# Optimization experiments

Hardware: AMD Instinct MI355X
Metric: run time of the kernel (lower is better)

Reference implementation:

```python
import jax, jax.numpy as jnp
import numpy as np

V, D, NL = 50257, 768, 12
DI, DS, DC, DTR = 1536, 16, 4, 48  # d_inner, d_state, d_conv, dt_rank
B, S = 2, 1024


def _mamba_layer(x, iw, cw, cb, xw, dw, db, Alog, Dp, ow):
    # x: (B,S,D)
    xz = x @ iw.T                      # (B,S,2*DI)
    xin, z = jnp.split(xz, 2, axis=-1)
    # depthwise causal conv over sequence
    xc = jax.lax.conv_general_dilated(
        jnp.transpose(xin, (0, 2, 1)), cw[:, None, :],
        window_strides=(1,), padding=[(DC - 1, 0)],
        feature_group_count=DI, dimension_numbers=('NCL', 'OIL', 'NCL'))
    xin = jax.nn.silu(jnp.transpose(xc, (0, 2, 1)) + cb)  # (B,S,DI)
    dbl = xin @ xw.T                   # (B,S,DTR+2*DS)
    dt, Bm, Cm = dbl[..., :DTR], dbl[..., DTR:DTR + DS], dbl[..., DTR + DS:]
    dt = jax.nn.softplus(dt @ dw.T + db)  # (B,S,DI)
    A = -jnp.exp(Alog)                 # (DI,DS)

    def step(h, inp):
        dt_t, B_t, C_t, x_t = inp      # (B,DI),(B,DS),(B,DS),(B,DI)
        h = h * jnp.exp(dt_t[:, :, None] * A) + (dt_t * x_t)[:, :, None] * B_t[:, None, :]
        y = jnp.einsum('bds,bs->bd', h, C_t)
        return h, y

    h0 = jnp.zeros((x.shape[0], DI, DS), dtype=x.dtype)
    xs = (jnp.transpose(dt, (1, 0, 2)), jnp.transpose(Bm, (1, 0, 2)),
          jnp.transpose(Cm, (1, 0, 2)), jnp.transpose(xin, (1, 0, 2)))
    _, ys = jax.lax.scan(step, h0, xs)
    y = jnp.transpose(ys, (1, 0, 2)) + xin * Dp  # (B,S,DI)
    y = y * jax.nn.silu(z)
    return y @ ow.T                    # (B,S,D)


def _layernorm(x, w, b):
    mu = jnp.mean(x, axis=-1, keepdims=True)
    var = jnp.mean(jnp.square(x - mu), axis=-1, keepdims=True)
    return (x - mu) * jax.lax.rsqrt(var + 1e-5) * w + b


def setup_inputs() -> dict:
    key = jax.random.key(0)
    ks = jax.random.split(key, 10)
    s = 0.02
    input_ids = jax.random.randint(ks[0], (B, S), 0, V)
    emb = jax.random.normal(ks[1], (V, D), jnp.float32) * s
    in_proj_w = jax.random.normal(ks[2], (NL, 2 * DI, D), jnp.float32) * s
    conv_w = jax.random.normal(ks[3], (NL, DI, DC), jnp.float32) * 0.2
    conv_b = jnp.zeros((NL, DI), jnp.float32)
    x_proj_w = jax.random.normal(ks[4], (NL, DTR + 2 * DS, DI), jnp.float32) * s
    dt_proj_w = jax.random.normal(ks[5], (NL, DI, DTR), jnp.float32) * (DTR ** -0.5)
    dt_proj_b = jax.random.normal(ks[6], (NL, DI), jnp.float32) * 0.1 - 4.0
    A_log = jnp.broadcast_to(jnp.log(jnp.arange(1, DS + 1, dtype=jnp.float32)), (NL, DI, DS)) + 0.0
    D_param = jnp.ones((NL, DI), jnp.float32)
    out_proj_w = jax.random.normal(ks[7], (NL, D, DI), jnp.float32) * s
    norm_w = jnp.ones((D,), jnp.float32)
    norm_b = jnp.zeros((D,), jnp.float32)
    return {"input_ids": input_ids, "emb": emb, "in_proj_w": in_proj_w,
            "conv_w": conv_w, "conv_b": conv_b, "x_proj_w": x_proj_w,
            "dt_proj_w": dt_proj_w, "dt_proj_b": dt_proj_b, "A_log": A_log,
            "D_param": D_param, "out_proj_w": out_proj_w,
            "norm_w": norm_w, "norm_b": norm_b}


def reference(input_ids, emb, in_proj_w, conv_w, conv_b, x_proj_w, dt_proj_w,
              dt_proj_b, A_log, D_param, out_proj_w, norm_w, norm_b):
    x = emb[input_ids] * (D ** 0.5)    # (B,S,D)
    for i in range(NL):
        x = _mamba_layer(x, in_proj_w[i], conv_w[i], conv_b[i], x_proj_w[i],
                         dt_proj_w[i], dt_proj_b[i], A_log[i], D_param[i], out_proj_w[i])
    x = _layernorm(x, norm_w, norm_b)
    return x @ emb.T                   # tied lm_head: (B,S,V)
```

## Files before the change

### kernel.cpp

```cpp
#include <hip/hip_runtime.h>
#include <hip/hip_bf16.h>

#define DI 1536
#define DS 16
#define DC 4
#define DTR 48
#define NB 2
#define SL 1024
#define DM 768
#define NLAYER 12
#define VOCAB 50257
#define ROWS (NB*SL)
#define CCH 32
#define CLEN (SL/CCH)
#define NBIG (DI+32)

typedef __attribute__((ext_vector_type(8))) short bf16x8;
typedef __attribute__((ext_vector_type(4))) short short4v;
typedef __attribute__((ext_vector_type(4))) float f32x4;

__device__ inline short f2bf(float f) {
    unsigned u = __builtin_bit_cast(unsigned, f);
    unsigned r = (u + 0x7fffu + ((u >> 16) & 1u)) >> 16;
    return (short)r;
}
__device__ inline float bf2f(unsigned short u) {
    unsigned x = ((unsigned)u) << 16;
    return __builtin_bit_cast(float, x);
}

__device__ __forceinline__ void gl_lds16(const void* g, void* l) {
    __builtin_amdgcn_global_load_lds(
        (const __attribute__((address_space(1))) unsigned int*)g,
        (__attribute__((address_space(3))) unsigned int*)l, 16, 0, 0);
}

__global__ __launch_bounds__(256) void cvt_bf16_k(const float* __restrict__ src,
                                                  unsigned short* __restrict__ dst,
                                                  int n4) {
    int i = blockIdx.x * 256 + threadIdx.x;
    if (i >= n4) return;
    float4 v = *reinterpret_cast<const float4*>(src + (size_t)i * 4);
    short4v o;
    o[0] = f2bf(v.x); o[1] = f2bf(v.y); o[2] = f2bf(v.z); o[3] = f2bf(v.w);
    *reinterpret_cast<short4v*>(dst + (size_t)i * 4) = o;
}

__global__ __launch_bounds__(256) void wc_k(
    const float* __restrict__ dtw_all,
    const float* __restrict__ xpw_all,
    unsigned short* __restrict__ wbig)
{
    int l = blockIdx.z;
    const float* dtw = dtw_all + (size_t)l * DI * DTR;
    const float* xpw = xpw_all + (size_t)l * 80 * DI;
    unsigned short* wb = wbig + (size_t)l * NBIG * DI;
    int tid = threadIdx.x;
    if (blockIdx.y == 12) {
        if (blockIdx.x == 0) {
            for (int idx = tid; idx < 32 * DI; idx += 256) {
                int rr = idx / DI, k = idx - rr * DI;
                wb[(size_t)(DI + rr) * DI + k] =
                    (unsigned short)f2bf(xpw[(size_t)(48 + rr) * DI + k]);
            }
        }
        return;
    }
    __shared__ float sd[128 * 48];
    __shared__ float sx[48 * 128];
    int d0 = blockIdx.y * 128, k0 = blockIdx.x * 128;
    for (int idx = tid; idx < 128 * 48; idx += 256) {
        int r = idx / 48, j = idx - r * 48;
        sd[idx] = dtw[(size_t)(d0 + r) * DTR + j];
    }
    for (int idx = tid; idx < 48 * 128; idx += 256) {
        int j = idx / 128, k = idx - j * 128;
        sx[idx] = xpw[(size_t)j * DI + k0 + k];
    }
    __syncthreads();
    int tx = tid & 15, ty = tid >> 4;
    float acc[8][8] = {};
    for (int j = 0; j < 48; ++j) {
        float a[8], w[8];
        #pragma unroll
        for (int i = 0; i < 8; ++i) a[i] = sd[(ty * 8 + i) * 48 + j];
        #pragma unroll
        for (int i = 0; i < 8; ++i) w[i] = sx[j * 128 + tx * 8 + i];
        #pragma unroll
        for (int i = 0; i < 8; ++i)
            #pragma unroll
            for (int jj = 0; jj < 8; ++jj)
                acc[i][jj] += a[i] * w[jj];
    }
    for (int i = 0; i < 8; ++i)
        for (int jj = 0; jj < 8; ++jj)
            wb[(size_t)(d0 + ty * 8 + i) * DI + k0 + tx * 8 + jj] =
                (unsigned short)f2bf(acc[i][jj]);
}

__global__ __launch_bounds__(256) void embed_k(const int* __restrict__ ids,
                                               const float* __restrict__ emb,
                                               unsigned short* __restrict__ xbf) {
    int i = blockIdx.x * 256 + threadIdx.x;
    if (i >= ROWS * (DM / 4)) return;
    int row = i / (DM / 4);
    int c4 = (i - row * (DM / 4)) * 4;
    float4 v = *reinterpret_cast<const float4*>(
        &emb[(size_t)ids[row] * DM + c4]);
    const float s = 27.712812921102035f;
    short4v o;
    o[0] = f2bf(v.x * s); o[1] = f2bf(v.y * s);
    o[2] = f2bf(v.z * s); o[3] = f2bf(v.w * s);
    *reinterpret_cast<short4v*>(&xbf[(size_t)row * DM + c4]) = o;
}

template<int MT, int NBUF, int OUT, bool NTST>
__global__ __launch_bounds__(256) void gemm_bf16(
    const unsigned short* __restrict__ A, int lda,
    const unsigned short* __restrict__ W, int ldw,
    float* __restrict__ C, unsigned short* __restrict__ Cbf, int ldc,
    int GY, int N, int K,
    const float* __restrict__ bias, float* __restrict__ aux)
{
    constexpr int BKT = 32;
    constexpr int CPR = BKT / 8;
    constexpr int ACA = (MT * CPR + 255) / 256;
    constexpr int ACW = 128 * CPR / 256;
    constexpr int ISS = ACA + ACW;
    constexpr int MFR = MT / 32;
    constexpr int BUFS = (MT + 128) * BKT;
    __shared__ __align__(16) short smem[NBUF * BUFS];

    const int tid  = threadIdx.x;
    const int lane = tid & 63;
    const int wid  = tid >> 6;
    const int wr   = wid >> 1, wc = wid & 1;

    const int nwg = gridDim.x;
    const int q = nwg >> 3, rm = nwg & 7;
    const int xcd = blockIdx.x & 7, bidx = blockIdx.x >> 3;
    const int wg = (xcd < rm ? xcd * (q + 1) : rm * (q + 1) + (xcd - rm) * q) + bidx;
    const int row0 = (wg % GY) * MT;
    const int col0 = (wg / GY) * 128;

    const unsigned short* gA[ACA];
    const unsigned short* gW[ACW];
    #pragma unroll
    for (int i = 0; i < ACA; ++i) {
        int cid = i * 256 + ((MT == 32) ? (tid & 127) : tid);
        int r = cid / CPR, c = cid % CPR;
        gA[i] = A + (size_t)(row0 + r) * lda + ((c ^ ((r >> 1) & 3)) * 8);
    }
    #pragma unroll
    for (int i = 0; i < ACW; ++i) {
        int cid = i * 256 + tid;
        int r = cid / CPR, c = cid % CPR;
        int rg = col0 + r; if (rg > N - 1) rg = N - 1;
        gW[i] = W + (size_t)rg * ldw + ((c ^ ((r >> 1) & 3)) * 8);
    }

    const int arow = (MT == 32 ? wr * 16 : wr * (MT / 2)) + (lane & 15);
    const int brow = wc * 64 + (lane & 15);
    const int szA = (arow >> 1) & 3;
    const int szB = (brow >> 1) & 3;
    const int hi = lane >> 4;

    auto STAGE = [&](int buf) {
        short* As = smem + buf * BUFS;
        short* Ws = As + MT * BKT;
        #pragma unroll
        for (int i = 0; i < ACA; ++i) {
            int cbase = (MT == 32) ? ((wid & 1) * 64) : (i * 256 + wid * 64);
            gl_lds16(gA[i], &As[cbase * 8]);
            gA[i] += BKT;
        }
        #pragma unroll
        for (int i = 0; i < ACW; ++i) {
            gl_lds16(gW[i], &Ws[(i * 256 + wid * 64) * 8]);
            gW[i] += BKT;
        }
    };

    f32x4 acc[MFR][4] = {};

    const int ntiles = K / BKT;
    #pragma unroll
    for (int p = 0; p < NBUF - 1; ++p) STAGE(p);

    for (int t = 0; t < ntiles; ++t) {
        const int next = t + NBUF - 1;
        if (next < ntiles) STAGE(next % NBUF);
        int ahead = ntiles - 1 - t;
        if (ahead > NBUF - 1) ahead = NBUF - 1;
        if (NBUF == 3 && ahead == 2)
            asm volatile("s_waitcnt vmcnt(%0)" :: "n"(2 * ISS) : "memory");
        else if (ahead == 1)
            asm volatile("s_waitcnt vmcnt(%0)" :: "n"(ISS) : "memory");
        else if (ahead == 0)
            asm volatile("s_waitcnt vmcnt(0)" ::: "memory");
        __builtin_amdgcn_sched_barrier(0);
        __builtin_amdgcn_s_barrier();

        const short* As = smem + (t % NBUF) * BUFS;
        const short* Ws = As + MT * BKT;
        bf16x8 a[MFR], b[4];
        #pragma unroll
        for (int mf = 0; mf < MFR; ++mf)
            a[mf] = *reinterpret_cast<const bf16x8*>(
                &As[(arow + mf * 16) * BKT + ((hi ^ szA) * 8)]);
        #pragma unroll
        for (int nf = 0; nf < 4; ++nf)
            b[nf] = *reinterpret_cast<const bf16x8*>(
                &Ws[(brow + nf * 16) * BKT + ((hi ^ szB) * 8)]);
        #pragma unroll
        for (int mf = 0; mf < MFR; ++mf)
            #pragma unroll
            for (int nf = 0; nf < 4; ++nf)
                acc[mf][nf] = __builtin_amdgcn_mfma_f32_16x16x32_bf16(
                    a[mf], b[nf], acc[mf][nf], 0, 0, 0);

        __builtin_amdgcn_s_barrier();
    }

    if (OUT == 0 && NTST) {
        __syncthreads();
        float* Cs = (float*)smem;
        #pragma unroll
        for (int mf = 0; mf < MFR; ++mf) {
            __syncthreads();
            #pragma unroll
            for (int nf = 0; nf < 4; ++nf) {
                #pragma unroll
                for (int j = 0; j < 4; ++j)
                    Cs[(wr * 16 + hi * 4 + j) * 132 + wc * 64 + nf * 16 + (lane & 15)]
                        = acc[mf][nf][j];
            }
            __syncthreads();
            #pragma unroll
            for (int rr = 0; rr < 8; ++rr) {
                int lrow = wid * 8 + rr;
                int grow = row0 + (lrow < 16 ? mf * 16 + lrow
                                             : (MT / 2) + mf * 16 + (lrow - 16));
                #pragma unroll
                for (int hf = 0; hf < 2; ++hf) {
                    int cc = col0 + hf * 64 + lane;
                    if (cc < N)
                        __builtin_nontemporal_store(
                            Cs[lrow * 132 + hf * 64 + lane],
                            &C[(size_t)grow * ldc + cc]);
                }
            }
        }
    } else {
        #pragma unroll
        for (int mf = 0; mf < MFR; ++mf) {
            #pragma unroll
            for (int nf = 0; nf < 4; ++nf) {
                int r  = row0 + (MT == 32 ? wr * 16 : wr * (MT / 2)) + mf * 16 + hi * 4;
                int cc = col0 + wc * 64 + nf * 16 + (lane & 15);
                if (cc < N) {
                    f32x4 d = acc[mf][nf];
                    if (OUT == 3) {
                        if (cc < DI) {
                            float bv = bias[cc];
                            #pragma unroll
                            for (int j = 0; j < 4; ++j) {
                                float v = d[j] + bv;
                                v = (v > 20.f) ? v : log1pf(__expf(v));
                                Cbf[(size_t)(r + j) * ldc + cc] = (unsigned short)f2bf(v);
                            }
                        } else {
                            #pragma unroll
                            for (int j = 0; j < 4; ++j)
                                aux[(size_t)(r + j) * 32 + (cc - DI)] = d[j];
                        }
                    } else if (OUT == 2) {
                        #pragma unroll
                        for (int j = 0; j < 4; ++j)
                            Cbf[(size_t)(r + j) * ldc + cc] = (unsigned short)f2bf(d[j]);
                    } else {
                        #pragma unroll
                        for (int j = 0; j < 4; ++j)
                            C[(size_t)(r + j) * ldc + cc] = d[j];
                    }
                }
            }
        }
    }
}

__global__ __launch_bounds__(256) void conv_silu_k(
    const unsigned short* __restrict__ xz, const float* __restrict__ cw,
    const float* __restrict__ cb, unsigned short* __restrict__ xinb)
{
    int i = blockIdx.x * 256 + threadIdx.x;
    if (i >= ROWS * (DI / 8)) return;
    int row = i / (DI / 8);
    int c = (i - row * (DI / 8)) * 8;
    int t = row & (SL - 1);
    int b = row >> 10;

    float4 wv[8];
    float accv[8];
    #pragma unroll
    for (int j = 0; j < 8; ++j) {
        wv[j] = *reinterpret_cast<const float4*>(&cw[(c + j) * DC]);
        accv[j] = cb[c + j];
    }
    const unsigned short* base = xz + ((size_t)(b * SL)) * (2 * DI) + c;
    #pragma unroll
    for (int k = 0; k < DC; ++k) {
        int tt = t + k - (DC - 1);
        if (tt >= 0) {
            bf16x8 v = *reinterpret_cast<const bf16x8*>(
                &base[(size_t)tt * (2 * DI)]);
            #pragma unroll
            for (int j = 0; j < 8; ++j)
                accv[j] += bf2f((unsigned short)v[j]) *
                           reinterpret_cast<const float*>(&wv[j])[k];
        }
    }
    bf16x8 o;
    #pragma unroll
    for (int j = 0; j < 8; ++j) {
        float v = accv[j] / (1.f + __expf(-accv[j]));
        o[j] = f2bf(v);
    }
    *reinterpret_cast<bf16x8*>(&xinb[(size_t)row * DI + c]) = o;
}

__global__ __launch_bounds__(256) void scan_phase1(
    const unsigned short* __restrict__ dt,
    const float* __restrict__ bc,
    const unsigned short* __restrict__ xin,
    const float* __restrict__ Alog,
    float* __restrict__ hend,
    float* __restrict__ eprod)
{
    int blk = blockIdx.x;
    int c = blk % CCH;
    int tmp = blk / CCH;
    int dblk = tmp % (DI / 16);
    int b = tmp / (DI / 16);
    int s = threadIdx.x & 15;
    int d = dblk * 16 + (threadIdx.x >> 4);
    float A = -__expf(Alog[d * DS + s]);
    float h = 0.f, P = 1.f;
    const int rowbase = b * SL + c * CLEN;
    #pragma unroll 4
    for (int t = 0; t < CLEN; ++t) {
        int r = rowbase + t;
        float dtv = bf2f(dt[(size_t)r * DI + d]);
        float xv  = bf2f(xin[(size_t)r * DI + d]);
        float Bv  = bc[(size_t)r * 32 + s];
        float e = __expf(dtv * A);
        h = h * e + dtv * xv * Bv;
        P *= e;
    }
    size_t idx = ((size_t)(b * CCH + c) * DI + d) * DS + s;
    hend[idx]  = h;
    eprod[idx] = P;
}

__global__ __launch_bounds__(256) void scan_phase3(
    const unsigned short* __restrict__ dt,
    const float* __restrict__ bc,
    const unsigned short* __restrict__ xin,
    const unsigned short* __restrict__ xz,
    const float* __restrict__ Alog,
    const float* __restrict__ Dp,
    const float* __restrict__ hend,
    const float* __restrict__ eprod,
    unsigned short* __restrict__ ybf)
{
    int blk = blockIdx.x;
    int c = blk % CCH;
    int tmp = blk / CCH;
    int dblk = tmp % (DI / 16);
    int b = tmp / (DI / 16);
    int s = threadIdx.x & 15;
    int d = dblk * 16 + (threadIdx.x >> 4);
    float A = -__expf(Alog[d * DS + s]);
    float Dv = Dp[d];

    float h = 0.f;
    const size_t pbase = ((size_t)b * CCH * DI + d) * DS + s;
    for (int j = 0; j < c; ++j) {
        size_t idx = pbase + (size_t)j * (DI * DS);
        h = h * eprod[idx] + hend[idx];
    }

    const int rowbase = b * SL + c * CLEN;
    #pragma unroll 2
    for (int t = 0; t < CLEN; ++t) {
        int r = rowbase + t;
        float dtv = bf2f(dt[(size_t)r * DI + d]);
        float xv  = bf2f(xin[(size_t)r * DI + d]);
        float Bv  = bc[(size_t)r * 32 + s];
        float Cv  = bc[(size_t)r * 32 + 16 + s];
        float e = __expf(dtv * A);
        h = h * e + dtv * xv * Bv;
        float p = h * Cv;
        p += __shfl_xor(p, 1, 64);
        p += __shfl_xor(p, 2, 64);
        p += __shfl_xor(p, 4, 64);
        p += __shfl_xor(p, 8, 64);
        if (s == 0) {
            float z = bf2f(xz[(size_t)r * (2 * DI) + DI + d]);
            float yv = (p + xv * Dv) * (z / (1.f + __expf(-z)));
            ybf[(size_t)r * DI + d] = (unsigned short)f2bf(yv);
        }
    }
}

__global__ __launch_bounds__(256) void ln_k(
    const unsigned short* __restrict__ x, const float* __restrict__ w,
    const float* __restrict__ b, unsigned short* __restrict__ o)
{
    int row = blockIdx.x;
    int tid = threadIdx.x;
    const unsigned short* xr = x + (size_t)row * DM;
    float v0 = bf2f(xr[tid]), v1 = bf2f(xr[tid + 256]), v2 = bf2f(xr[tid + 512]);
    float s = v0 + v1 + v2;
    #pragma unroll
    for (int off = 1; off < 64; off <<= 1) s += __shfl_xor(s, off, 64);
    __shared__ float red[4];
    __shared__ float red2[4];
    int wid = tid >> 6, lane = tid & 63;
    if (lane == 0) red[wid] = s;
    __syncthreads();
    float mu = (red[0] + red[1] + red[2] + red[3]) * (1.f / 768.f);
    float d0 = v0 - mu, d1 = v1 - mu, d2 = v2 - mu;
    float q = d0 * d0 + d1 * d1 + d2 * d2;
    #pragma unroll
    for (int off = 1; off < 64; off <<= 1) q += __shfl_xor(q, off, 64);
    if (lane == 0) red2[wid] = q;
    __syncthreads();
    float var = (red2[0] + red2[1] + red2[2] + red2[3]) * (1.f / 768.f);
    float rs = rsqrtf(var + 1e-5f);
    o[(size_t)row * DM + tid]       = (unsigned short)f2bf(d0 * rs * w[tid]       + b[tid]);
    o[(size_t)row * DM + tid + 256] = (unsigned short)f2bf(d1 * rs * w[tid + 256] + b[tid + 256]);
    o[(size_t)row * DM + tid + 512] = (unsigned short)f2bf(d2 * rs * w[tid + 512] + b[tid + 512]);
}

extern "C" void kernel_launch(void* const* d_in, const int* in_sizes, int n_in,
                              void* d_out, int out_size, void* d_ws, size_t ws_size,
                              hipStream_t stream) {
    const int*   ids        = (const int*)d_in[0];
    const float* emb        = (const float*)d_in[1];
    const float* in_proj_w  = (const float*)d_in[2];
    const float* conv_w     = (const float*)d_in[3];
    const float* conv_b     = (const float*)d_in[4];
    const float* x_proj_w   = (const float*)d_in[5];
    const float* dt_proj_w  = (const float*)d_in[6];
    const float* dt_proj_b  = (const float*)d_in[7];
    const float* A_log      = (const float*)d_in[8];
    const float* D_param    = (const float*)d_in[9];
    const float* out_proj_w = (const float*)d_in[10];
    const float* norm_w     = (const float*)d_in[11];
    const float* norm_b     = (const float*)d_in[12];
    float* out = (float*)d_out;

    char* base = (char*)d_ws;
    size_t off = 0;
    auto alloc_f = [&](size_t n) { float* p = (float*)(base + off); off += n * 4; return p; };
    auto alloc_u = [&](size_t n) { unsigned short* p = (unsigned short*)(base + off); off += n * 2; return p; };

    float* bc    = alloc_f((size_t)ROWS * 32);
    float* hend  = alloc_f((size_t)NB * CCH * DI * DS);
    float* eprod = alloc_f((size_t)NB * CCH * DI * DS);
    unsigned short* xbf   = alloc_u((size_t)ROWS * DM);
    unsigned short* xzb   = alloc_u((size_t)ROWS * 2 * DI);
    unsigned short* xinb  = alloc_u((size_t)ROWS * DI);
    unsigned short* dtbf  = alloc_u((size_t)ROWS * DI);
    unsigned short* ybf   = alloc_u((size_t)ROWS * DI);
    unsigned short* xlnbf = alloc_u((size_t)ROWS * DM);
    unsigned short* inw_bf = alloc_u((size_t)NLAYER * 2 * DI * DM);
    unsigned short* ow_bf  = alloc_u((size_t)NLAYER * DM * DI);
    unsigned short* wbig  = alloc_u((size_t)NLAYER * NBIG * DI);
    unsigned short* emb_bf = alloc_u((size_t)VOCAB * DM);
    (void)ws_size;

    {
        int n4a = NLAYER * 2 * DI * DM / 4;
        cvt_bf16_k<<<(n4a + 255) / 256, 256, 0, stream>>>(in_proj_w, inw_bf, n4a);
        int n4b = NLAYER * DM * DI / 4;
        cvt_bf16_k<<<(n4b + 255) / 256, 256, 0, stream>>>(out_proj_w, ow_bf, n4b);
        wc_k<<<dim3(12, 13, NLAYER), 256, 0, stream>>>(dt_proj_w, x_proj_w, wbig);
        int n4e = VOCAB * DM / 4;
        cvt_bf16_k<<<(n4e + 255) / 256, 256, 0, stream>>>(emb, emb_bf, n4e);
    }

    embed_k<<<(ROWS * (DM / 4) + 255) / 256, 256, 0, stream>>>(ids, emb, xbf);

    const int scan_grid = NB * (DI / 16) * CCH;

    for (int i = 0; i < NLAYER; ++i) {
        const float* cw  = conv_w  + (size_t)i * DI * DC;
        const float* cb  = conv_b  + (size_t)i * DI;
        const float* dtb = dt_proj_b + (size_t)i * DI;
        const float* Al  = A_log   + (size_t)i * DI * DS;
        const float* Dpar= D_param + (size_t)i * DI;

        const unsigned short* inw = inw_bf + (size_t)i * 2 * DI * DM;
        gemm_bf16<64, 3, 2, false><<<24 * 32, 256, 0, stream>>>(
            xbf, DM, inw, DM, nullptr, xzb, 2 * DI, 32, 2 * DI, DM, nullptr, nullptr);

        conv_silu_k<<<(ROWS * (DI / 8)) / 256, 256, 0, stream>>>(xzb, cw, cb, xinb);

        const unsigned short* wb = wbig + (size_t)i * NBIG * DI;
        gemm_bf16<64, 3, 3, false><<<13 * 32, 256, 0, stream>>>(
            xinb, DI, wb, DI, nullptr, dtbf, DI, 32, NBIG, DI, dtb, bc);

        scan_phase1<<<scan_grid, 256, 0, stream>>>(dtbf, bc, xinb, Al, hend, eprod);
        scan_phase3<<<scan_grid, 256, 0, stream>>>(dtbf, bc, xinb, xzb, Al, Dpar,
                                                   hend, eprod, ybf);

        const unsigned short* ow = ow_bf + (size_t)i * DM * DI;
        gemm_bf16<32, 3, 2, false><<<64 * 6, 256, 0, stream>>>(
            ybf, DI, ow, DI, nullptr, xbf, DM, 64, DM, DI, nullptr, nullptr);
    }

    ln_k<<<ROWS, 256, 0, stream>>>(xbf, norm_w, norm_b, xlnbf);
    gemm_bf16<128, 2, 0, true><<<393 * 16, 256, 0, stream>>>(
        xlnbf, DM, emb_bf, DM, out, nullptr, VOCAB, 16, VOCAB, DM, nullptr, nullptr);
}
```

Measured before the change: 3.130 ms.

## Widen lm_head GEMM tile, shuffle-broadcast scan inputs, merge weight conversions

The GEMM kernel gains an NCOL template parameter, and the final vocabulary projection now uses 128x256 tiles to raise reuse of the A operand, at the cost of more accumulator registers and LDS. Both scan phases now load dt, x and z once per 16 timesteps, one value per lane, and broadcast them with wave shuffles instead of having all 16 state lanes reload the same values each step. The three fp32-to-bf16 weight conversion launches are merged into a single kernel to cut launch overhead.

```diff
diff --git a/kernel.cpp b/kernel.cpp
--- a/kernel.cpp
+++ b/kernel.cpp
@@ -35,11 +35,17 @@
         (__attribute__((address_space(3))) unsigned int*)l, 16, 0, 0);
 }
 
-__global__ __launch_bounds__(256) void cvt_bf16_k(const float* __restrict__ src,
-                                                  unsigned short* __restrict__ dst,
-                                                  int n4) {
+__global__ __launch_bounds__(256) void cvt3_k(
+    const float* __restrict__ s0, unsigned short* __restrict__ d0, int n40,
+    const float* __restrict__ s1, unsigned short* __restrict__ d1, int n41,
+    const float* __restrict__ s2, unsigned short* __restrict__ d2, int n42)
+{
     int i = blockIdx.x * 256 + threadIdx.x;
-    if (i >= n4) return;
+    const float* src; unsigned short* dst;
+    if (i < n40) { src = s0; dst = d0; }
+    else if (i < n40 + n41) { i -= n40; src = s1; dst = d1; }
+    else if (i < n40 + n41 + n42) { i -= n40 + n41; src = s2; dst = d2; }
+    else return;
     float4 v = *reinterpret_cast<const float4*>(src + (size_t)i * 4);
     short4v o;
     o[0] = f2bf(v.x); o[1] = f2bf(v.y); o[2] = f2bf(v.z); o[3] = f2bf(v.w);
@@ -114,7 +120,7 @@
     *reinterpret_cast<short4v*>(&xbf[(size_t)row * DM + c4]) = o;
 }
 
-template<int MT, int NBUF, int OUT, bool NTST>
+template<int MT, int NCOL, int NBUF, int OUT, bool NTST>
 __global__ __launch_bounds__(256) void gemm_bf16(
     const unsigned short* __restrict__ A, int lda,
     const unsigned short* __restrict__ W, int ldw,
@@ -125,10 +131,11 @@
     constexpr int BKT = 32;
     constexpr int CPR = BKT / 8;
     constexpr int ACA = (MT * CPR + 255) / 256;
-    constexpr int ACW = 128 * CPR / 256;
+    constexpr int ACW = NCOL * CPR / 256;
     constexpr int ISS = ACA + ACW;
     constexpr int MFR = MT / 32;
-    constexpr int BUFS = (MT + 128) * BKT;
+    constexpr int NFR = NCOL / 32;
+    constexpr int BUFS = (MT + NCOL) * BKT;
     __shared__ __align__(16) short smem[NBUF * BUFS];
 
     const int tid  = threadIdx.x;
@@ -141,7 +148,7 @@
     const int xcd = blockIdx.x & 7, bidx = blockIdx.x >> 3;
     const int wg = (xcd < rm ? xcd * (q + 1) : rm * (q + 1) + (xcd - rm) * q) + bidx;
     const int row0 = (wg % GY) * MT;
-    const int col0 = (wg / GY) * 128;
+    const int col0 = (wg / GY) * NCOL;
 
     const unsigned short* gA[ACA];
     const unsigned short* gW[ACW];
@@ -160,7 +167,7 @@
     }
 
     const int arow = (MT == 32 ? wr * 16 : wr * (MT / 2)) + (lane & 15);
-    const int brow = wc * 64 + (lane & 15);
+    const int brow = wc * (NCOL / 2) + (lane & 15);
     const int szA = (arow >> 1) & 3;
     const int szB = (brow >> 1) & 3;
     const int hi = lane >> 4;
@@ -181,7 +188,7 @@
         }
     };
 
-    f32x4 acc[MFR][4] = {};
+    f32x4 acc[MFR][NFR] = {};
 
     const int ntiles = K / BKT;
     #pragma unroll
@@ -203,19 +210,19 @@
 
         const short* As = smem + (t % NBUF) * BUFS;
         const short* Ws = As + MT * BKT;
-        bf16x8 a[MFR], b[4];
+        bf16x8 a[MFR], b[NFR];
         #pragma unroll
         for (int mf = 0; mf < MFR; ++mf)
             a[mf] = *reinterpret_cast<const bf16x8*>(
                 &As[(arow + mf * 16) * BKT + ((hi ^ szA) * 8)]);
         #pragma unroll
-        for (int nf = 0; nf < 4; ++nf)
+        for (int nf = 0; nf < NFR; ++nf)
             b[nf] = *reinterpret_cast<const bf16x8*>(
                 &Ws[(brow + nf * 16) * BKT + ((hi ^ szB) * 8)]);
         #pragma unroll
         for (int mf = 0; mf < MFR; ++mf)
             #pragma unroll
-            for (int nf = 0; nf < 4; ++nf)
+            for (int nf = 0; nf < NFR; ++nf)
                 acc[mf][nf] = __builtin_amdgcn_mfma_f32_16x16x32_bf16(
                     a[mf], b[nf], acc[mf][nf], 0, 0, 0);
 
@@ -224,15 +231,16 @@
 
     if (OUT == 0 && NTST) {
         __syncthreads();
+        constexpr int CSLD = NCOL + 4;
         float* Cs = (float*)smem;
         #pragma unroll
         for (int mf = 0; mf < MFR; ++mf) {
             __syncthreads();
             #pragma unroll
-            for (int nf = 0; nf < 4; ++nf) {
+            for (int nf = 0; nf < NFR; ++nf) {
                 #pragma unroll
                 for (int j = 0; j < 4; ++j)
-                    Cs[(wr * 16 + hi * 4 + j) * 132 + wc * 64 + nf * 16 + (lane & 15)]
+                    Cs[(wr * 16 + hi * 4 + j) * CSLD + wc * (NCOL / 2) + nf * 16 + (lane & 15)]
                         = acc[mf][nf][j];
             }
             __syncthreads();
@@ -242,11 +250,11 @@
                 int grow = row0 + (lrow < 16 ? mf * 16 + lrow
                                              : (MT / 2) + mf * 16 + (lrow - 16));
                 #pragma unroll
-                for (int hf = 0; hf < 2; ++hf) {
+                for (int hf = 0; hf < NCOL / 64; ++hf) {
                     int cc = col0 + hf * 64 + lane;
                     if (cc < N)
                         __builtin_nontemporal_store(
-                            Cs[lrow * 132 + hf * 64 + lane],
+                            Cs[lrow * CSLD + hf * 64 + lane],
                             &C[(size_t)grow * ldc + cc]);
                 }
             }
@@ -255,9 +263,9 @@
         #pragma unroll
         for (int mf = 0; mf < MFR; ++mf) {
             #pragma unroll
-            for (int nf = 0; nf < 4; ++nf) {
+            for (int nf = 0; nf < NFR; ++nf) {
                 int r  = row0 + (MT == 32 ? wr * 16 : wr * (MT / 2)) + mf * 16 + hi * 4;
-                int cc = col0 + wc * 64 + nf * 16 + (lane & 15);
+                int cc = col0 + wc * (NCOL / 2) + nf * 16 + (lane & 15);
                 if (cc < N) {
                     f32x4 d = acc[mf][nf];
                     if (OUT == 3) {
@@ -342,20 +350,28 @@
     int tmp = blk / CCH;
     int dblk = tmp % (DI / 16);
     int b = tmp / (DI / 16);
-    int s = threadIdx.x & 15;
+    int lane = threadIdx.x & 63;
+    int s = lane & 15;
+    int g = lane & 0x30;
     int d = dblk * 16 + (threadIdx.x >> 4);
     float A = -__expf(Alog[d * DS + s]);
     float h = 0.f, P = 1.f;
     const int rowbase = b * SL + c * CLEN;
-    #pragma unroll 4
-    for (int t = 0; t < CLEN; ++t) {
-        int r = rowbase + t;
-        float dtv = bf2f(dt[(size_t)r * DI + d]);
-        float xv  = bf2f(xin[(size_t)r * DI + d]);
-        float Bv  = bc[(size_t)r * 32 + s];
-        float e = __expf(dtv * A);
-        h = h * e + dtv * xv * Bv;
-        P *= e;
+    #pragma unroll
+    for (int half = 0; half < 2; ++half) {
+        int rb = rowbase + half * 16;
+        int rl = rb + s;
+        float dtv_b = bf2f(dt[(size_t)rl * DI + d]);
+        float xv_b  = bf2f(xin[(size_t)rl * DI + d]);
+        #pragma unroll
+        for (int t = 0; t < 16; ++t) {
+            float dtv = __shfl(dtv_b, g | t, 64);
+            float xv  = __shfl(xv_b,  g | t, 64);
+            float Bv  = bc[(size_t)(rb + t) * 32 + s];
+            float e = __expf(dtv * A);
+            h = h * e + dtv * xv * Bv;
+            P *= e;
+        }
     }
     size_t idx = ((size_t)(b * CCH + c) * DI + d) * DS + s;
     hend[idx]  = h;
@@ -378,7 +394,9 @@
     int tmp = blk / CCH;
     int dblk = tmp % (DI / 16);
     int b = tmp / (DI / 16);
-    int s = threadIdx.x & 15;
+    int lane = threadIdx.x & 63;
+    int s = lane & 15;
+    int g = lane & 0x30;
     int d = dblk * 16 + (threadIdx.x >> 4);
     float A = -__expf(Alog[d * DS + s]);
     float Dv = Dp[d];
@@ -391,24 +409,32 @@
     }
 
     const int rowbase = b * SL + c * CLEN;
-    #pragma unroll 2
-    for (int t = 0; t < CLEN; ++t) {
-        int r = rowbase + t;
-        float dtv = bf2f(dt[(size_t)r * DI + d]);
-        float xv  = bf2f(xin[(size_t)r * DI + d]);
-        float Bv  = bc[(size_t)r * 32 + s];
-        float Cv  = bc[(size_t)r * 32 + 16 + s];
-        float e = __expf(dtv * A);
-        h = h * e + dtv * xv * Bv;
-        float p = h * Cv;
-        p += __shfl_xor(p, 1, 64);
-        p += __shfl_xor(p, 2, 64);
-        p += __shfl_xor(p, 4, 64);
-        p += __shfl_xor(p, 8, 64);
-        if (s == 0) {
-            float z = bf2f(xz[(size_t)r * (2 * DI) + DI + d]);
-            float yv = (p + xv * Dv) * (z / (1.f + __expf(-z)));
-            ybf[(size_t)r * DI + d] = (unsigned short)f2bf(yv);
+    #pragma unroll
+    for (int half = 0; half < 2; ++half) {
+        int rb = rowbase + half * 16;
+        int rl = rb + s;
+        float dtv_b = bf2f(dt[(size_t)rl * DI + d]);
+        float xv_b  = bf2f(xin[(size_t)rl * DI + d]);
+        float zv_b  = bf2f(xz[(size_t)rl * (2 * DI) + DI + d]);
+        #pragma unroll
+        for (int t = 0; t < 16; ++t) {
+            float dtv = __shfl(dtv_b, g | t, 64);
+            float xv  = __shfl(xv_b,  g | t, 64);
+            int r = rb + t;
+            float Bv  = bc[(size_t)r * 32 + s];
+            float Cv  = bc[(size_t)r * 32 + 16 + s];
+            float e = __expf(dtv * A);
+            h = h * e + dtv * xv * Bv;
+            float p = h * Cv;
+            p += __shfl_xor(p, 1, 64);
+            p += __shfl_xor(p, 2, 64);
+            p += __shfl_xor(p, 4, 64);
+            p += __shfl_xor(p, 8, 64);
+            float z = __shfl(zv_b, g | t, 64);
+            if (s == 0) {
+                float yv = (p + xv * Dv) * (z / (1.f + __expf(-z)));
+                ybf[(size_t)r * DI + d] = (unsigned short)f2bf(yv);
+            }
         }
     }
 }
@@ -483,12 +509,12 @@
 
     {
         int n4a = NLAYER * 2 * DI * DM / 4;
-        cvt_bf16_k<<<(n4a + 255) / 256, 256, 0, stream>>>(in_proj_w, inw_bf, n4a);
         int n4b = NLAYER * DM * DI / 4;
-        cvt_bf16_k<<<(n4b + 255) / 256, 256, 0, stream>>>(out_proj_w, ow_bf, n4b);
+        int n4e = VOCAB * DM / 4;
+        int n4t = n4a + n4b + n4e;
+        cvt3_k<<<(n4t + 255) / 256, 256, 0, stream>>>(
+            in_proj_w, inw_bf, n4a, out_proj_w, ow_bf, n4b, emb, emb_bf, n4e);
         wc_k<<<dim3(12, 13, NLAYER), 256, 0, stream>>>(dt_proj_w, x_proj_w, wbig);
-        int n4e = VOCAB * DM / 4;
-        cvt_bf16_k<<<(n4e + 255) / 256, 256, 0, stream>>>(emb, emb_bf, n4e);
     }
 
     embed_k<<<(ROWS * (DM / 4) + 255) / 256, 256, 0, stream>>>(ids, emb, xbf);
@@ -503,13 +529,13 @@
         const float* Dpar= D_param + (size_t)i * DI;
 
         const unsigned short* inw = inw_bf + (size_t)i * 2 * DI * DM;
-        gemm_bf16<64, 3, 2, false><<<24 * 32, 256, 0, stream>>>(
+        gemm_bf16<64, 128, 3, 2, false><<<24 * 32, 256, 0, stream>>>(
             xbf, DM, inw, DM, nullptr, xzb, 2 * DI, 32, 2 * DI, DM, nullptr, nullptr);
 
         conv_silu_k<<<(ROWS * (DI / 8)) / 256, 256, 0, stream>>>(xzb, cw, cb, xinb);
 
         const unsigned short* wb = wbig + (size_t)i * NBIG * DI;
-        gemm_bf16<64, 3, 3, false><<<13 * 32, 256, 0, stream>>>(
+        gemm_bf16<64, 128, 3, 3, false><<<13 * 32, 256, 0, stream>>>(
             xinb, DI, wb, DI, nullptr, dtbf, DI, 32, NBIG, DI, dtb, bc);
 
         scan_phase1<<<scan_grid, 256, 0, stream>>>(dtbf, bc, xinb, Al, hend, eprod);
@@ -517,11 +543,11 @@
                                                    hend, eprod, ybf);
 
         const unsigned short* ow = ow_bf + (size_t)i * DM * DI;
-        gemm_bf16<32, 3, 2, false><<<64 * 6, 256, 0, stream>>>(
+        gemm_bf16<32, 128, 3, 2, false><<<64 * 6, 256, 0, stream>>>(
             ybf, DI, ow, DI, nullptr, xbf, DM, 64, DM, DI, nullptr, nullptr);
     }
 
     ln_k<<<ROWS, 256, 0, stream>>>(xbf, norm_w, norm_b, xlnbf);
-    gemm_bf16<128, 2, 0, true><<<393 * 16, 256, 0, stream>>>(
+    gemm_bf16<128, 256, 2, 0, true><<<197 * 16, 256, 0, stream>>>(
         xlnbf, DM, emb_bf, DM, out, nullptr, VOCAB, 16, VOCAB, DM, nullptr, nullptr);
 }
```

Result: faster. 2.947 ms (-5.9%).
